# Kernel tuning notes

Hardware: AMD Instinct MI355X
Metric: run time of the kernel (lower is better)

## Reference

```python
import jax, jax.numpy as jnp
import numpy as np

KERNEL_SIZE = 3   # init kwarg kernel_size
BATCHSIZE = 4     # init kwarg batchsize (true output batch; bs = num * BATCHSIZE)


def setup_inputs() -> dict:
    key = jax.random.key(0)
    k1, k2, k3 = jax.random.split(key, 3)
    num = 4                      # candidate flows per image
    bs = num * BATCHSIZE         # 16
    ds, hs, ws = 256, 64, 64
    hf, wf = 64, 64
    source = jax.random.normal(k1, (bs, ds, hs, ws), dtype=jnp.float32)
    # flows with realistic magnitude (a few pixels of displacement)
    flow_field = jax.random.normal(k2, (bs, 2, hf, wf), dtype=jnp.float32) * 8.0
    masks = jax.random.uniform(k3, (bs, 1, hf, wf), dtype=jnp.float32)
    return {"source": source, "flow_field": flow_field, "masks": masks}


def _bilinear_sample_zero(img, y, x):
    """img: (C,H,W); y,x: (Ho,Wo) continuous coords. Zero outside bounds."""
    C, H, W = img.shape
    y0 = jnp.floor(y).astype(jnp.int32)
    x0 = jnp.floor(x).astype(jnp.int32)
    out = jnp.zeros((C,) + y.shape, img.dtype)
    for dy in (0, 1):
        for dx in (0, 1):
            yi = y0 + dy
            xi = x0 + dx
            w = (1.0 - jnp.abs(y - yi)) * (1.0 - jnp.abs(x - xi))
            valid = (yi >= 0) & (yi < H) & (xi >= 0) & (xi < W)
            v = img[:, jnp.clip(yi, 0, H - 1), jnp.clip(xi, 0, W - 1)]  # (C,Ho,Wo)
            out = out + jnp.where(valid, w, 0.0)[None] * v
    return out


def reference(source, flow_field, masks):
    k, B = KERNEL_SIZE, BATCHSIZE
    bs, ds, hs, ws = source.shape
    hf, wf = flow_field.shape[2], flow_field.shape[3]
    num = bs // B
    Ho, Wo = k * hf, k * wf

    ys = jnp.arange(Ho)
    xs = jnp.arange(Wo)
    ysrc = ys // k              # which flow cell each output row belongs to
    xsrc = xs // k
    yoff = (ys % k) - (k // 2)  # centered in-block offset
    xoff = (xs % k) - (k // 2)

    # expand per-cell flow to per-output-pixel: (bs, Ho, Wo)
    fy = flow_field[:, 0][:, ysrc][:, :, xsrc]
    fx = flow_field[:, 1][:, ysrc][:, :, xsrc]
    py = ysrc.astype(fy.dtype)[:, None] + yoff.astype(fy.dtype)[:, None] + fy
    px = xsrc.astype(fx.dtype)[None, :] + xoff.astype(fx.dtype)[None, :] + fx

    sampled = jax.vmap(_bilinear_sample_zero)(source, py, px)  # (bs, ds, Ho, Wo)

    # per-cell mask broadcast over the kxk block and channels
    m = masks[:, :, ysrc][:, :, :, xsrc]  # (bs, 1, Ho, Wo)
    weighted = sampled * m

    # accumulate the num candidate flows into the true batch
    out = weighted.reshape(num, B, ds, Ho, Wo).sum(axis=0)
    return out
```

## Files before the change

kernel.cpp:

```cpp
#include <hip/hip_runtime.h>

#define DS 256
#define HS 64
#define WS 64
#define BOUT 4
#define NUM 4
#define HO 192
#define WO 192
#define NTHREADS 512
#define IMG_FLOATS (NUM * HS * WS)
#define LDS_FLOATS (IMG_FLOATS + 8)

__global__ __launch_bounds__(NTHREADS, 4)
void mbe_kernel(const float* __restrict__ src,
                const float* __restrict__ flow,
                const float* __restrict__ masks,
                float* __restrict__ out)
{
    extern __shared__ float lds[];
    float* img = lds + 4;

    const int d  = blockIdx.x;
    const int bo = blockIdx.y;
    const int tid = threadIdx.x;

    #pragma unroll
    for (int n = 0; n < NUM; ++n) {
        const float4* g = (const float4*)(src + (((size_t)(n * BOUT + bo) * DS + d) * (size_t)(HS * WS)));
        float4* s = (float4*)(img + n * (HS * WS));
        #pragma unroll
        for (int it = 0; it < 2; ++it)
            s[it * NTHREADS + tid] = g[it * NTHREADS + tid];
    }
    __syncthreads();

    const size_t obase = ((size_t)bo * DS + d) * (size_t)(HO * WO);

    for (int it = 0; it < 8; ++it) {
        const int g  = it * NTHREADS + tid;
        const int ys = g >> 6;
        const int xs = g & 63;

        float fy[NUM], fx[NUM], mm[NUM];
        #pragma unroll
        for (int n = 0; n < NUM; ++n) {
            const int b = n * BOUT + bo;
            fy[n] = flow[((size_t)(b * 2 + 0) << 12) + g];
            fx[n] = flow[((size_t)(b * 2 + 1) << 12) + g];
            mm[n] = masks[((size_t)b << 12) + g];
        }

        float acc[3][3];
        #pragma unroll
        for (int j = 0; j < 3; ++j)
            #pragma unroll
            for (int i = 0; i < 3; ++i)
                acc[j][i] = 0.0f;

        #pragma unroll
        for (int n = 0; n < NUM; ++n) {
            const float gy = (float)ys + fy[n];
            const float gx = (float)xs + fx[n];
            const float fiy = floorf(gy);
            const float fix = floorf(gx);
            const int iy = (int)fiy;
            const int ix = (int)fix;
            const float ty = gy - fiy;
            const float tx = gx - fix;

            const int ixm1 = ix - 1;
            const int ixc  = min(max(ixm1, -3), 63);
            bool xv[4];
            #pragma unroll
            for (int c = 0; c < 4; ++c)
                xv[c] = ((unsigned)(ixm1 + c) < (unsigned)WS);

            const float* imgn = img + n * (HS * WS);

            float hx[4][3];
            #pragma unroll
            for (int r = 0; r < 4; ++r) {
                const int yy = iy - 1 + r;
                const bool yv = ((unsigned)yy < (unsigned)HS);
                const int yyc = min(max(yy, 0), HS - 1);
                const float* p = imgn + yyc * WS + ixc;
                float v[4];
                #pragma unroll
                for (int c = 0; c < 4; ++c) {
                    const float lv = p[c];
                    v[c] = (yv & xv[c]) ? lv : 0.0f;
                }
                #pragma unroll
                for (int i = 0; i < 3; ++i)
                    hx[r][i] = v[i] + tx * (v[i + 1] - v[i]);
            }

            const float wy1 = mm[n] * ty;
            const float wy0 = mm[n] - wy1;
            #pragma unroll
            for (int j = 0; j < 3; ++j)
                #pragma unroll
                for (int i = 0; i < 3; ++i)
                    acc[j][i] += wy0 * hx[j][i] + wy1 * hx[j + 1][i];
        }

        #pragma unroll
        for (int j = 0; j < 3; ++j) {
            const int yo = 3 * ys + j;
            #pragma unroll
            for (int i = 0; i < 3; ++i) {
                const int xo = 3 * xs + i;
                out[obase + (size_t)yo * WO + xo] = acc[j][i];
            }
        }
    }
}

extern "C" void kernel_launch(void* const* d_in, const int* in_sizes, int n_in,
                              void* d_out, int out_size, void* d_ws, size_t ws_size,
                              hipStream_t stream) {
    const float* src   = (const float*)d_in[0];
    const float* flow  = (const float*)d_in[1];
    const float* masks = (const float*)d_in[2];
    float* out = (float*)d_out;

    const size_t shmem = LDS_FLOATS * sizeof(float);
    static bool attr_set = false;
    if (!attr_set) {
        hipFuncSetAttribute((const void*)mbe_kernel,
                            hipFuncAttributeMaxDynamicSharedMemorySize, (int)shmem);
        attr_set = true;
    }

    dim3 grid(DS, BOUT);
    mbe_kernel<<<grid, NTHREADS, shmem, stream>>>(src, flow, masks, out);
}
```

Baseline: 237.0 us.

## Store source tile in LDS as packed bf16 with padded rows and weight-folded bounds

Converts the staged source planes to bf16 packed in pairs, with zero-padded rows, so the per-block LDS footprint halves (64KB to about 36KB) and launch bounds can allow more resident blocks. Each bilinear row fetch becomes two 64-bit LDS loads plus alignbit extraction instead of four scalar loads. Boundary handling is folded into the interpolation weights rather than masking the loaded values. The rounding to bf16 loses precision relative to the fp32 reference and may exceed tolerance; the extra unpacking ALU could also offset the LDS savings.

Result: slower. 309.8 us (+30.7%).

```diff
diff --git a/kernel.cpp b/kernel.cpp
--- a/kernel.cpp
+++ b/kernel.cpp
@@ -7,37 +7,56 @@
 #define NUM 4
 #define HO 192
 #define WO 192
-#define NTHREADS 512
-#define IMG_FLOATS (NUM * HS * WS)
-#define LDS_FLOATS (IMG_FLOATS + 8)
+#define NT 512
+#define ROWDW 36
+#define IMGDW (HS * ROWDW)
 
-__global__ __launch_bounds__(NTHREADS, 4)
+__device__ __forceinline__ unsigned int f2bf(float f) {
+    unsigned int u = __float_as_uint(f);
+    return (u + 0x7fffu + ((u >> 16) & 1u)) >> 16;
+}
+
+__global__ __launch_bounds__(NT, 8)
 void mbe_kernel(const float* __restrict__ src,
                 const float* __restrict__ flow,
                 const float* __restrict__ masks,
                 float* __restrict__ out)
 {
-    extern __shared__ float lds[];
-    float* img = lds + 4;
+    __shared__ unsigned int img[NUM * IMGDW];
 
     const int d  = blockIdx.x;
     const int bo = blockIdx.y;
     const int tid = threadIdx.x;
 
+    if (tid < NUM * HS) {
+        const int n = tid >> 6, row = tid & 63;
+        unsigned int* rb = img + n * IMGDW + row * ROWDW;
+        *(uint2*)rb        = make_uint2(0u, 0u);
+        *(uint2*)(rb + 34) = make_uint2(0u, 0u);
+    }
+
     #pragma unroll
-    for (int n = 0; n < NUM; ++n) {
-        const float4* g = (const float4*)(src + (((size_t)(n * BOUT + bo) * DS + d) * (size_t)(HS * WS)));
-        float4* s = (float4*)(img + n * (HS * WS));
-        #pragma unroll
-        for (int it = 0; it < 2; ++it)
-            s[it * NTHREADS + tid] = g[it * NTHREADS + tid];
+    for (int l = 0; l < 4; ++l) {
+        const int s = l * NT + tid;
+        const int n = s >> 9, row = (s >> 3) & 63, seg = s & 7;
+        const float* g = src + (((size_t)((n * BOUT + bo) * DS + d)) << 12) + (row << 6) + (seg << 3);
+        const float4 a = *(const float4*)g;
+        const float4 b = *(const float4*)(g + 4);
+        const unsigned int p0 = f2bf(a.x) | (f2bf(a.y) << 16);
+        const unsigned int p1 = f2bf(a.z) | (f2bf(a.w) << 16);
+        const unsigned int p2 = f2bf(b.x) | (f2bf(b.y) << 16);
+        const unsigned int p3 = f2bf(b.z) | (f2bf(b.w) << 16);
+        unsigned int* dst = img + n * IMGDW + row * ROWDW + 2 + (seg << 2);
+        *(uint2*)dst       = make_uint2(p0, p1);
+        *(uint2*)(dst + 2) = make_uint2(p2, p3);
     }
     __syncthreads();
 
     const size_t obase = ((size_t)bo * DS + d) * (size_t)(HO * WO);
 
+    #pragma unroll 1
     for (int it = 0; it < 8; ++it) {
-        const int g  = it * NTHREADS + tid;
+        const int g  = it * NT + tid;
         const int ys = g >> 6;
         const int xs = g & 63;
 
@@ -68,40 +87,63 @@
             const float ty = gy - fiy;
             const float tx = gx - fix;
 
-            const int ixm1 = ix - 1;
-            const int ixc  = min(max(ixm1, -3), 63);
-            bool xv[4];
-            #pragma unroll
-            for (int c = 0; c < 4; ++c)
-                xv[c] = ((unsigned)(ixm1 + c) < (unsigned)WS);
+            const int xb = ix - 1;
+            int c0 = xb & ~3;
+            c0 = min(max(c0, -4), 60);
+            const int r = xb - c0;
+            const bool rhi = (r >= 2);
+            const unsigned int sh = (unsigned int)((r & 1) << 4);
 
-            const float* imgn = img + n * (HS * WS);
-
-            float hx[4][3];
-            #pragma unroll
-            for (int r = 0; r < 4; ++r) {
-                const int yy = iy - 1 + r;
-                const bool yv = ((unsigned)yy < (unsigned)HS);
-                const int yyc = min(max(yy, 0), HS - 1);
-                const float* p = imgn + yyc * WS + ixc;
-                float v[4];
-                #pragma unroll
-                for (int c = 0; c < 4; ++c) {
-                    const float lv = p[c];
-                    v[c] = (yv & xv[c]) ? lv : 0.0f;
-                }
-                #pragma unroll
-                for (int i = 0; i < 3; ++i)
-                    hx[r][i] = v[i] + tx * (v[i + 1] - v[i]);
-            }
+            const float omtx = 1.0f - tx;
+            const float A0 = ((unsigned)xb       < (unsigned)WS) ? omtx : 0.0f;
+            const float A1 = ((unsigned)(xb + 1) < (unsigned)WS) ? omtx : 0.0f;
+            const float A2 = ((unsigned)(xb + 2) < (unsigned)WS) ? omtx : 0.0f;
+            const float B0 = ((unsigned)(xb + 1) < (unsigned)WS) ? tx : 0.0f;
+            const float B1 = ((unsigned)(xb + 2) < (unsigned)WS) ? tx : 0.0f;
+            const float B2 = ((unsigned)(xb + 3) < (unsigned)WS) ? tx : 0.0f;
 
             const float wy1 = mm[n] * ty;
             const float wy0 = mm[n] - wy1;
+            float WA[3], WB[3];
             #pragma unroll
-            for (int j = 0; j < 3; ++j)
-                #pragma unroll
-                for (int i = 0; i < 3; ++i)
-                    acc[j][i] += wy0 * hx[j][i] + wy1 * hx[j + 1][i];
+            for (int j = 0; j < 3; ++j) {
+                WA[j] = ((unsigned)(iy - 1 + j) < (unsigned)HS) ? wy0 : 0.0f;
+                WB[j] = ((unsigned)(iy + j)     < (unsigned)HS) ? wy1 : 0.0f;
+            }
+
+            const unsigned int* imgn = img + n * IMGDW;
+            const int cdw = (c0 >> 1) + 2;
+
+            #pragma unroll
+            for (int rr = 0; rr < 4; ++rr) {
+                const int yy = iy - 1 + rr;
+                const int yyc = min(max(yy, 0), HS - 1);
+                const unsigned int* p = imgn + yyc * ROWDW + cdw;
+                const uint2 u01 = *(const uint2*)p;
+                const uint2 u23 = *(const uint2*)(p + 2);
+                const unsigned int X = rhi ? u01.y : u01.x;
+                const unsigned int Y = rhi ? u23.x : u01.y;
+                const unsigned int Z = rhi ? u23.y : u23.x;
+                const unsigned int A = __builtin_amdgcn_alignbit(Y, X, sh);
+                const unsigned int B = __builtin_amdgcn_alignbit(Z, Y, sh);
+                const float v0 = __uint_as_float(A << 16);
+                const float v1 = __uint_as_float(A & 0xffff0000u);
+                const float v2 = __uint_as_float(B << 16);
+                const float v3 = __uint_as_float(B & 0xffff0000u);
+                const float h0 = v0 * A0 + v1 * B0;
+                const float h1 = v1 * A1 + v2 * B1;
+                const float h2 = v2 * A2 + v3 * B2;
+                if (rr <= 2) {
+                    acc[rr][0] += WA[rr] * h0;
+                    acc[rr][1] += WA[rr] * h1;
+                    acc[rr][2] += WA[rr] * h2;
+                }
+                if (rr >= 1) {
+                    acc[rr - 1][0] += WB[rr - 1] * h0;
+                    acc[rr - 1][1] += WB[rr - 1] * h1;
+                    acc[rr - 1][2] += WB[rr - 1] * h2;
+                }
+            }
         }
 
         #pragma unroll
@@ -124,14 +166,6 @@
     const float* masks = (const float*)d_in[2];
     float* out = (float*)d_out;
 
-    const size_t shmem = LDS_FLOATS * sizeof(float);
-    static bool attr_set = false;
-    if (!attr_set) {
-        hipFuncSetAttribute((const void*)mbe_kernel,
-                            hipFuncAttributeMaxDynamicSharedMemorySize, (int)shmem);
-        attr_set = true;
-    }
-
     dim3 grid(DS, BOUT);
-    mbe_kernel<<<grid, NTHREADS, shmem, stream>>>(src, flow, masks, out);
+    mbe_kernel<<<grid, NT, 0, stream>>>(src, flow, masks, out);
 }
```
